# Optimization experiments

Measured on AMD Instinct MI355X. Metric: run time of the kernel, lower is better.

The kernel has to match this reference:

```python
import jax, jax.numpy as jnp
import numpy as np

OUT_F, IN_F, N = 8192, 8192, 16

def setup_inputs() -> dict:
    key = jax.random.key(0)
    k1, k2 = jax.random.split(key)
    x = jax.random.normal(k1, (IN_F, N), dtype=jnp.float32)
    # symmetric int8 weights stored as int8 (quantized per-tensor)
    int8_weights = jax.random.randint(k2, (OUT_F, IN_F), -128, 128, dtype=jnp.int8)
    # power-of-two per-tensor scale, as produced by derive_int8_quant_parameters
    scaler = jnp.float32(2.0 ** -7)
    return {"x": x, "int8_weights": int8_weights, "scaler": scaler}

def reference(x, int8_weights, scaler):
    # dequant_weight: cast int8 -> fp32, multiply by per-tensor scaler
    fp_weights = int8_weights.astype(jnp.float32) * scaler  # [out, in]
    # forward: activation = W @ x  (weight on the left, x is [in, N])
    activation = jnp.matmul(fp_weights, x)  # [out, N]
    return activation
```

## Files before the change

kernel.cpp:

```cpp
#include <hip/hip_runtime.h>

typedef _Float16 half8 __attribute__((ext_vector_type(8)));
typedef float floatx4 __attribute__((ext_vector_type(4)));

constexpr int IN_F  = 8192;
constexpr int OUT_F = 8192;
constexpr int NCOL  = 16;

constexpr int CHUNKS  = 32;
constexpr int CHUNK_K = IN_F / CHUNKS;
constexpr int STEPS   = CHUNK_K / 32;
constexpr int RB      = 4;
constexpr int WPB     = 4;
constexpr int ROWS_PER_WAVE = RB * 16;
constexpr int RGROUPS = OUT_F / ROWS_PER_WAVE;
constexpr int NBLOCKS = CHUNKS * RGROUPS / WPB;

__global__ __launch_bounds__(256, 4)
void lq_mfma_kernel(const float* __restrict__ x,
                    const void* __restrict__ wraw,
                    const float* __restrict__ scaler,
                    float* __restrict__ out)
{
    const int tid   = threadIdx.x;
    const int lane  = tid & 63;
    const int wv    = tid >> 6;
    const int W     = blockIdx.x * WPB + wv;
    const int chunk = W & (CHUNKS - 1);
    const int rg    = W / CHUNKS;
    const int k0    = chunk * CHUNK_K;
    const int m     = lane & 15;
    const int quad  = lane >> 4;

    const int* wi = (const int*)wraw;
    bool w_is_i32 = true;
    #pragma unroll
    for (int i = 0; i < 16; ++i) {
        int v = wi[i];
        w_is_i32 = w_is_i32 && (v >= -128) && (v <= 127);
    }

    const float s = *scaler;

    half8 bf[STEPS];
    #pragma unroll
    for (int st = 0; st < STEPS; ++st) {
        #pragma unroll
        for (int j = 0; j < 8; ++j) {
            const int k = k0 + st * 32 + quad * 8 + j;
            bf[st][j] = (_Float16)x[k * NCOL + m];
        }
    }

    if (w_is_i32) {
        const int* wp = (const int*)wraw;
        #pragma unroll 1
        for (int r = 0; r < RB; ++r) {
            const int row = rg * ROWS_PER_WAVE + r * 16 + m;
            const int* wrow = wp + (size_t)row * IN_F + k0 + quad * 8;
            floatx4 acc = {0.f, 0.f, 0.f, 0.f};
            #pragma unroll
            for (int st = 0; st < STEPS; ++st) {
                half8 af;
                #pragma unroll
                for (int j = 0; j < 8; ++j)
                    af[j] = (_Float16)wrow[st * 32 + j];
                acc = __builtin_amdgcn_mfma_f32_16x16x32_f16(af, bf[st], acc, 0, 0, 0);
            }
            const int orow = rg * ROWS_PER_WAVE + r * 16 + quad * 4;
            #pragma unroll
            for (int g = 0; g < 4; ++g)
                atomicAdd(&out[(orow + g) * NCOL + m], acc[g] * s);
        }
    } else {
        const signed char* wp = (const signed char*)wraw;
        #pragma unroll 1
        for (int r = 0; r < RB; ++r) {
            const int row = rg * ROWS_PER_WAVE + r * 16 + m;
            const signed char* wrow = wp + (size_t)row * IN_F + k0 + quad * 8;
            floatx4 acc = {0.f, 0.f, 0.f, 0.f};
            #pragma unroll
            for (int st = 0; st < STEPS; ++st) {
                const uint2 u = *(const uint2*)(wrow + st * 32);
                half8 af;
                #pragma unroll
                for (int j = 0; j < 4; ++j) {
                    af[j]     = (_Float16)(int)(signed char)(u.x >> (8 * j));
                    af[j + 4] = (_Float16)(int)(signed char)(u.y >> (8 * j));
                }
                acc = __builtin_amdgcn_mfma_f32_16x16x32_f16(af, bf[st], acc, 0, 0, 0);
            }
            const int orow = rg * ROWS_PER_WAVE + r * 16 + quad * 4;
            #pragma unroll
            for (int g = 0; g < 4; ++g)
                atomicAdd(&out[(orow + g) * NCOL + m], acc[g] * s);
        }
    }
}

extern "C" void kernel_launch(void* const* d_in, const int* in_sizes, int n_in,
                              void* d_out, int out_size, void* d_ws, size_t ws_size,
                              hipStream_t stream)
{
    const float* x      = (const float*)d_in[0];
    const void*  w      = d_in[1];
    const float* scaler = (const float*)d_in[2];
    float*       out    = (float*)d_out;

    hipMemsetAsync(out, 0, (size_t)OUT_F * NCOL * sizeof(float), stream);
    lq_mfma_kernel<<<NBLOCKS, 256, 0, stream>>>(x, w, scaler, out);
}
```

Baseline: 374.5 us.

## Replace atomic split-K accumulation with partial buffers and a reduce kernel

Each K-chunk wave now writes its partial 16-column results to its own slice of a workspace buffer instead of atomically adding into the output. A second kernel sums the 32 partials, applies the scale and writes the output, which also removes the memset. Weight loads are batched into wide vector loads up front so more memory requests are in flight. In exchange the workspace adds about 16 MB of partial writes plus reads and a second launch.

```diff
diff --git a/kernel.cpp b/kernel.cpp
--- a/kernel.cpp
+++ b/kernel.cpp
@@ -15,12 +15,12 @@
 constexpr int ROWS_PER_WAVE = RB * 16;
 constexpr int RGROUPS = OUT_F / ROWS_PER_WAVE;
 constexpr int NBLOCKS = CHUNKS * RGROUPS / WPB;
+constexpr size_t PART_STRIDE = (size_t)OUT_F * NCOL;
 
 __global__ __launch_bounds__(256, 4)
 void lq_mfma_kernel(const float* __restrict__ x,
                     const void* __restrict__ wraw,
-                    const float* __restrict__ scaler,
-                    float* __restrict__ out)
+                    float* __restrict__ part)
 {
     const int tid   = threadIdx.x;
     const int lane  = tid & 63;
@@ -40,8 +40,6 @@
         w_is_i32 = w_is_i32 && (v >= -128) && (v <= 127);
     }
 
-    const float s = *scaler;
-
     half8 bf[STEPS];
     #pragma unroll
     for (int st = 0; st < STEPS; ++st) {
@@ -52,50 +50,81 @@
         }
     }
 
+    float* pbase = part + (size_t)chunk * PART_STRIDE;
+
     if (w_is_i32) {
         const int* wp = (const int*)wraw;
         #pragma unroll 1
         for (int r = 0; r < RB; ++r) {
             const int row = rg * ROWS_PER_WAVE + r * 16 + m;
-            const int* wrow = wp + (size_t)row * IN_F + k0 + quad * 8;
+            const uint4* wrow = (const uint4*)(wp + (size_t)row * IN_F + k0 + quad * 8);
+            uint4 raw[2 * STEPS];
+            #pragma unroll
+            for (int st = 0; st < STEPS; ++st) {
+                raw[2 * st]     = wrow[8 * st];
+                raw[2 * st + 1] = wrow[8 * st + 1];
+            }
             floatx4 acc = {0.f, 0.f, 0.f, 0.f};
             #pragma unroll
             for (int st = 0; st < STEPS; ++st) {
                 half8 af;
+                const int* p0 = (const int*)&raw[2 * st];
                 #pragma unroll
                 for (int j = 0; j < 8; ++j)
-                    af[j] = (_Float16)wrow[st * 32 + j];
+                    af[j] = (_Float16)p0[j];
                 acc = __builtin_amdgcn_mfma_f32_16x16x32_f16(af, bf[st], acc, 0, 0, 0);
             }
             const int orow = rg * ROWS_PER_WAVE + r * 16 + quad * 4;
             #pragma unroll
             for (int g = 0; g < 4; ++g)
-                atomicAdd(&out[(orow + g) * NCOL + m], acc[g] * s);
+                pbase[(size_t)(orow + g) * NCOL + m] = acc[g];
         }
     } else {
         const signed char* wp = (const signed char*)wraw;
         #pragma unroll 1
         for (int r = 0; r < RB; ++r) {
             const int row = rg * ROWS_PER_WAVE + r * 16 + m;
-            const signed char* wrow = wp + (size_t)row * IN_F + k0 + quad * 8;
+            const uint2* wrow = (const uint2*)(wp + (size_t)row * IN_F + k0 + quad * 8);
+            uint2 raw[STEPS];
+            #pragma unroll
+            for (int st = 0; st < STEPS; ++st)
+                raw[st] = wrow[4 * st];
             floatx4 acc = {0.f, 0.f, 0.f, 0.f};
             #pragma unroll
             for (int st = 0; st < STEPS; ++st) {
-                const uint2 u = *(const uint2*)(wrow + st * 32);
                 half8 af;
                 #pragma unroll
                 for (int j = 0; j < 4; ++j) {
-                    af[j]     = (_Float16)(int)(signed char)(u.x >> (8 * j));
-                    af[j + 4] = (_Float16)(int)(signed char)(u.y >> (8 * j));
+                    af[j]     = (_Float16)(int)(signed char)(raw[st].x >> (8 * j));
+                    af[j + 4] = (_Float16)(int)(signed char)(raw[st].y >> (8 * j));
                 }
                 acc = __builtin_amdgcn_mfma_f32_16x16x32_f16(af, bf[st], acc, 0, 0, 0);
             }
             const int orow = rg * ROWS_PER_WAVE + r * 16 + quad * 4;
             #pragma unroll
             for (int g = 0; g < 4; ++g)
-                atomicAdd(&out[(orow + g) * NCOL + m], acc[g] * s);
+                pbase[(size_t)(orow + g) * NCOL + m] = acc[g];
         }
     }
+}
+
+__global__ __launch_bounds__(256)
+void lq_reduce_kernel(const float* __restrict__ part,
+                      const float* __restrict__ scaler,
+                      float* __restrict__ out)
+{
+    const int i = blockIdx.x * blockDim.x + threadIdx.x;
+    const float4* p = (const float4*)part;
+    const int stride = (int)(PART_STRIDE / 4);
+    float4 a = p[i];
+    #pragma unroll
+    for (int c = 1; c < CHUNKS; ++c) {
+        float4 v = p[(size_t)c * stride + i];
+        a.x += v.x; a.y += v.y; a.z += v.z; a.w += v.w;
+    }
+    const float s = *scaler;
+    float4 r = {a.x * s, a.y * s, a.z * s, a.w * s};
+    ((float4*)out)[i] = r;
 }
 
 extern "C" void kernel_launch(void* const* d_in, const int* in_sizes, int n_in,
@@ -106,7 +135,8 @@
     const void*  w      = d_in[1];
     const float* scaler = (const float*)d_in[2];
     float*       out    = (float*)d_out;
+    float*       part   = (float*)d_ws;
 
-    hipMemsetAsync(out, 0, (size_t)OUT_F * NCOL * sizeof(float), stream);
-    lq_mfma_kernel<<<NBLOCKS, 256, 0, stream>>>(x, w, scaler, out);
+    lq_mfma_kernel<<<NBLOCKS, 256, 0, stream>>>(x, w, part);
+    lq_reduce_kernel<<<(OUT_F * NCOL / 4) / 256, 256, 0, stream>>>(part, scaler, out);
 }
```

After: 378.9 us. About the same (+1.2%).
